# Kernel optimization log

Measured on AMD Instinct MI355X. Metric: run time of the kernel, lower is better.

Reference implementation:

```python
import jax, jax.numpy as jnp
import numpy as np

N_NODES = 100000
N_EDGES = 1600000
H_FEATS = 64


def setup_inputs() -> dict:
    key = jax.random.key(0)
    k_h, k_src, k_dst, k_w1, k_b1, k_w2, k_b2 = jax.random.split(key, 7)
    h = jax.random.normal(k_h, (N_NODES, H_FEATS), dtype=jnp.float32)
    src = jax.random.randint(k_src, (N_EDGES,), 0, N_NODES, dtype=jnp.int64)
    dst = jax.random.randint(k_dst, (N_EDGES,), 0, N_NODES, dtype=jnp.int64)
    # Linear params (torch Linear: y = x @ W.T + b). Store as [in, out] for jnp.
    lim1 = 1.0 / np.sqrt(2 * H_FEATS)
    W1 = jax.random.uniform(k_w1, (2 * H_FEATS, H_FEATS), minval=-lim1, maxval=lim1, dtype=jnp.float32)
    b1 = jax.random.uniform(k_b1, (H_FEATS,), minval=-lim1, maxval=lim1, dtype=jnp.float32)
    lim2 = 1.0 / np.sqrt(H_FEATS)
    W2 = jax.random.uniform(k_w2, (H_FEATS, 1), minval=-lim2, maxval=lim2, dtype=jnp.float32)
    b2 = jax.random.uniform(k_b2, (1,), minval=-lim2, maxval=lim2, dtype=jnp.float32)
    return {"h": h, "src": src, "dst": dst, "W1": W1, "b1": b1, "W2": W2, "b2": b2}


def reference(h, src, dst, W1, b1, W2, b2):
    # Gather src/dst node features per edge, avoid materializing the concat by
    # splitting W1 into the src-half and dst-half of the contraction.
    W1s, W1d = W1[:H_FEATS], W1[H_FEATS:]            # each [h, h]
    h_src = h[src]                                    # [E, h]
    h_dst = h[dst]                                    # [E, h]
    hidden = jax.nn.relu(h_src @ W1s + h_dst @ W1d + b1)  # [E, h]
    score = (hidden @ W2 + b2)[:, 0]                  # [E]
    return score
```

## Files before the change

kernel.cpp:

```cpp
#include <hip/hip_runtime.h>
#include <hip/hip_fp16.h>


#define HF  64
#define PAD 65
#define TN  128

__global__ __launch_bounds__(512) void node_proj_kernel(
    const float* __restrict__ h, const float* __restrict__ W1,
    const float* __restrict__ b1, __half* __restrict__ P,
    __half* __restrict__ Q, int n_nodes)
{
    __shared__ float hs[TN * PAD];

    const int tid  = threadIdx.x;
    const int lane = tid & 63;
    const int wave = __builtin_amdgcn_readfirstlane(tid >> 6);
    const int c0   = wave * 16;
    const bool isQ = c0 >= 64;
    const int ccol = c0 & 63;

    const float* wbase = W1 + (isQ ? (HF * HF) : 0) + ccol;
    __half* const outh = (isQ ? Q : P) + ccol;

    const int n0 = blockIdx.x * TN;

    {
        const int nrow  = (n_nodes - n0 < TN) ? (n_nodes - n0) : TN;
        const int maxf4 = nrow * 16;
        const float4* hv = (const float4*)(h + (size_t)n0 * HF);
        #pragma unroll
        for (int it = 0; it < 4; ++it) {
            const int idx  = tid + it * 512;
            const int cidx = (idx < maxf4) ? idx : 0;
            const float4 v = hv[cidx];
            const int row = idx >> 4;
            const int c4  = (idx & 15) * 4;
            float* dst = &hs[row * PAD + c4];
            dst[0] = v.x; dst[1] = v.y; dst[2] = v.z; dst[3] = v.w;
        }
    }
    __syncthreads();

    float acc0[16], acc1[16];
    #pragma unroll
    for (int j = 0; j < 16; ++j) {
        const float b = isQ ? 0.0f : b1[ccol + j];
        acc0[j] = b; acc1[j] = b;
    }

    const float* r0 = &hs[lane * PAD];
    const float* r1 = &hs[(lane + 64) * PAD];

    #pragma unroll 4
    for (int k2 = 0; k2 < 32; ++k2) {
        const float a0 = r0[2 * k2], a1 = r0[2 * k2 + 1];
        const float c0v = r1[2 * k2], c1v = r1[2 * k2 + 1];
        const float* wA = wbase + (2 * k2) * HF;
        const float* wB = wbase + (2 * k2 + 1) * HF;
        #pragma unroll
        for (int j = 0; j < 16; ++j) {
            const float wa = wA[j], wb = wB[j];
            acc0[j] = fmaf(a0, wa, acc0[j]);
            acc0[j] = fmaf(a1, wb, acc0[j]);
            acc1[j] = fmaf(c0v, wa, acc1[j]);
            acc1[j] = fmaf(c1v, wb, acc1[j]);
        }
    }

    const int n_a = n0 + lane;
    const int n_b = n0 + lane + 64;
    if (n_a < n_nodes) {
        union { uint4 u[2]; __half2 hh[8]; } pk;
        #pragma unroll
        for (int j = 0; j < 8; ++j)
            pk.hh[j] = __floats2half2_rn(acc0[2 * j], acc0[2 * j + 1]);
        __half* base = outh + (size_t)n_a * HF;
        *(uint4*)(base)     = pk.u[0];
        *(uint4*)(base + 8) = pk.u[1];
    }
    if (n_b < n_nodes) {
        union { uint4 u[2]; __half2 hh[8]; } pk;
        #pragma unroll
        for (int j = 0; j < 8; ++j)
            pk.hh[j] = __floats2half2_rn(acc1[2 * j], acc1[2 * j + 1]);
        __half* base = outh + (size_t)n_b * HF;
        *(uint4*)(base)     = pk.u[0];
        *(uint4*)(base + 8) = pk.u[1];
    }
}

__device__ __forceinline__ float dot8_relu(uint4 pv, uint4 qv, float4 wa, float4 wb) {
    const __half2* ph = (const __half2*)&pv;
    const __half2* qh = (const __half2*)&qv;
    const float2 p0 = __half22float2(ph[0]), q0 = __half22float2(qh[0]);
    const float2 p1 = __half22float2(ph[1]), q1 = __half22float2(qh[1]);
    const float2 p2 = __half22float2(ph[2]), q2 = __half22float2(qh[2]);
    const float2 p3 = __half22float2(ph[3]), q3 = __half22float2(qh[3]);
    float acc = 0.f;
    acc = fmaf(fmaxf(p0.x + q0.x, 0.f), wa.x, acc);
    acc = fmaf(fmaxf(p0.y + q0.y, 0.f), wa.y, acc);
    acc = fmaf(fmaxf(p1.x + q1.x, 0.f), wa.z, acc);
    acc = fmaf(fmaxf(p1.y + q1.y, 0.f), wa.w, acc);
    acc = fmaf(fmaxf(p2.x + q2.x, 0.f), wb.x, acc);
    acc = fmaf(fmaxf(p2.y + q2.y, 0.f), wb.y, acc);
    acc = fmaf(fmaxf(p3.x + q3.x, 0.f), wb.z, acc);
    acc = fmaf(fmaxf(p3.y + q3.y, 0.f), wb.w, acc);
    return acc;
}

__device__ __forceinline__ float red8(float v) {
    v += __shfl_xor(v, 4, 8);
    v += __shfl_xor(v, 2, 8);
    v += __shfl_xor(v, 1, 8);
    return v;
}

__global__ __launch_bounds__(256) void edge_score_kernel(
    const __half* __restrict__ P, const __half* __restrict__ Q,
    const int* __restrict__ src, const int* __restrict__ dst,
    const float* __restrict__ W2, const float* __restrict__ b2,
    float* __restrict__ out, int n_edges)
{
    const int tid   = blockIdx.x * 256 + threadIdx.x;
    const int sub   = threadIdx.x & 7;
    const int group = tid >> 3;
    const int j0    = sub * 8;
    const int e0    = group * 8;
    if (e0 >= n_edges) return;

    const float4 w2a = *(const float4*)(W2 + j0);
    const float4 w2b = *(const float4*)(W2 + j0 + 4);
    const float bias2 = b2[0];

    if (e0 + 8 <= n_edges) {
        const int4 sA = *(const int4*)(src + e0);
        const int4 sB = *(const int4*)(src + e0 + 4);
        const int4 dA = *(const int4*)(dst + e0);
        const int4 dB = *(const int4*)(dst + e0 + 4);

        const uint4 p0 = *(const uint4*)(P + (size_t)sA.x * HF + j0);
        const uint4 p1 = *(const uint4*)(P + (size_t)sA.y * HF + j0);
        const uint4 p2 = *(const uint4*)(P + (size_t)sA.z * HF + j0);
        const uint4 p3 = *(const uint4*)(P + (size_t)sA.w * HF + j0);
        const uint4 p4 = *(const uint4*)(P + (size_t)sB.x * HF + j0);
        const uint4 p5 = *(const uint4*)(P + (size_t)sB.y * HF + j0);
        const uint4 p6 = *(const uint4*)(P + (size_t)sB.z * HF + j0);
        const uint4 p7 = *(const uint4*)(P + (size_t)sB.w * HF + j0);
        const uint4 q0 = *(const uint4*)(Q + (size_t)dA.x * HF + j0);
        const uint4 q1 = *(const uint4*)(Q + (size_t)dA.y * HF + j0);
        const uint4 q2 = *(const uint4*)(Q + (size_t)dA.z * HF + j0);
        const uint4 q3 = *(const uint4*)(Q + (size_t)dA.w * HF + j0);
        const uint4 q4 = *(const uint4*)(Q + (size_t)dB.x * HF + j0);
        const uint4 q5 = *(const uint4*)(Q + (size_t)dB.y * HF + j0);
        const uint4 q6 = *(const uint4*)(Q + (size_t)dB.z * HF + j0);
        const uint4 q7 = *(const uint4*)(Q + (size_t)dB.w * HF + j0);

        float s0 = red8(dot8_relu(p0, q0, w2a, w2b));
        float s1 = red8(dot8_relu(p1, q1, w2a, w2b));
        float s2 = red8(dot8_relu(p2, q2, w2a, w2b));
        float s3 = red8(dot8_relu(p3, q3, w2a, w2b));
        float s4 = red8(dot8_relu(p4, q4, w2a, w2b));
        float s5 = red8(dot8_relu(p5, q5, w2a, w2b));
        float s6 = red8(dot8_relu(p6, q6, w2a, w2b));
        float s7 = red8(dot8_relu(p7, q7, w2a, w2b));

        if (sub == 0) {
            *(float4*)(out + e0)     = make_float4(s0 + bias2, s1 + bias2,
                                                   s2 + bias2, s3 + bias2);
            *(float4*)(out + e0 + 4) = make_float4(s4 + bias2, s5 + bias2,
                                                   s6 + bias2, s7 + bias2);
        }
    } else {
        for (int e = e0; e < n_edges; ++e) {
            const int s = src[e];
            const int d = dst[e];
            const uint4 pv = *(const uint4*)(P + (size_t)s * HF + j0);
            const uint4 qv = *(const uint4*)(Q + (size_t)d * HF + j0);
            float sc = red8(dot8_relu(pv, qv, w2a, w2b));
            if (sub == 0) out[e] = sc + bias2;
        }
    }
}

extern "C" void kernel_launch(void* const* d_in, const int* in_sizes, int n_in,
                              void* d_out, int out_size, void* d_ws, size_t ws_size,
                              hipStream_t stream) {
    const float* h   = (const float*)d_in[0];
    const int*   src = (const int*)d_in[1];
    const int*   dst = (const int*)d_in[2];
    const float* W1  = (const float*)d_in[3];
    const float* b1  = (const float*)d_in[4];
    const float* W2  = (const float*)d_in[5];
    const float* b2  = (const float*)d_in[6];
    float* out = (float*)d_out;

    const int n_nodes = in_sizes[0] / HF;
    const int n_edges = in_sizes[1];

    __half* P = (__half*)d_ws;
    __half* Q = P + (size_t)n_nodes * HF;

    const int nblocks1 = (n_nodes + TN - 1) / TN;
    node_proj_kernel<<<nblocks1, 512, 0, stream>>>(h, W1, b1, P, Q, n_nodes);

    const int ngroups  = (n_edges + 7) / 8;
    const int nblocks2 = (ngroups + 31) / 32;
    edge_score_kernel<<<nblocks2, 256, 0, stream>>>(P, Q, src, dst, W2, b2, out, n_edges);
}
```

Measured before the change: 156.2 us.

## Halve node tile, cache h row in registers, vectorize LDS accesses

The node projection kernel now handles 64 nodes per block instead of 128, so each lane owns one node and one set of 16 accumulators. The full 64-float h row is loaded into registers with float4 LDS reads, using a padding of 68 so the float4 accesses stay aligned, and the k loop is fully unrolled. This removes the scalar LDS reads and doubles the block count for more parallelism. In exchange it raises register pressure and halves the reuse of each W1 load across nodes. The edge kernel, which likely dominates runtime, is unchanged.

```diff
diff --git a/kernel.cpp b/kernel.cpp
--- a/kernel.cpp
+++ b/kernel.cpp
@@ -3,8 +3,8 @@
 
 
 #define HF  64
-#define PAD 65
-#define TN  128
+#define TN  64
+#define PAD 68
 
 __global__ __launch_bounds__(512) void node_proj_kernel(
     const float* __restrict__ h, const float* __restrict__ W1,
@@ -23,68 +23,56 @@
     const float* wbase = W1 + (isQ ? (HF * HF) : 0) + ccol;
     __half* const outh = (isQ ? Q : P) + ccol;
 
-    const int n0 = blockIdx.x * TN;
+    const int n0   = blockIdx.x * TN;
+    const int nrow = (n_nodes - n0 < TN) ? (n_nodes - n0) : TN;
 
     {
-        const int nrow  = (n_nodes - n0 < TN) ? (n_nodes - n0) : TN;
         const int maxf4 = nrow * 16;
         const float4* hv = (const float4*)(h + (size_t)n0 * HF);
         #pragma unroll
-        for (int it = 0; it < 4; ++it) {
+        for (int it = 0; it < 2; ++it) {
             const int idx  = tid + it * 512;
             const int cidx = (idx < maxf4) ? idx : 0;
             const float4 v = hv[cidx];
             const int row = idx >> 4;
             const int c4  = (idx & 15) * 4;
-            float* dst = &hs[row * PAD + c4];
-            dst[0] = v.x; dst[1] = v.y; dst[2] = v.z; dst[3] = v.w;
+            *(float4*)&hs[row * PAD + c4] = v;
         }
     }
     __syncthreads();
 
-    float acc0[16], acc1[16];
-    #pragma unroll
-    for (int j = 0; j < 16; ++j) {
-        const float b = isQ ? 0.0f : b1[ccol + j];
-        acc0[j] = b; acc1[j] = b;
-    }
-
-    const float* r0 = &hs[lane * PAD];
-    const float* r1 = &hs[(lane + 64) * PAD];
-
-    #pragma unroll 4
-    for (int k2 = 0; k2 < 32; ++k2) {
-        const float a0 = r0[2 * k2], a1 = r0[2 * k2 + 1];
-        const float c0v = r1[2 * k2], c1v = r1[2 * k2 + 1];
-        const float* wA = wbase + (2 * k2) * HF;
-        const float* wB = wbase + (2 * k2 + 1) * HF;
+    float hreg[64];
+    {
+        const float* r = &hs[lane * PAD];
         #pragma unroll
-        for (int j = 0; j < 16; ++j) {
-            const float wa = wA[j], wb = wB[j];
-            acc0[j] = fmaf(a0, wa, acc0[j]);
-            acc0[j] = fmaf(a1, wb, acc0[j]);
-            acc1[j] = fmaf(c0v, wa, acc1[j]);
-            acc1[j] = fmaf(c1v, wb, acc1[j]);
+        for (int k4 = 0; k4 < 16; ++k4) {
+            const float4 v = *(const float4*)(r + k4 * 4);
+            hreg[k4 * 4 + 0] = v.x;
+            hreg[k4 * 4 + 1] = v.y;
+            hreg[k4 * 4 + 2] = v.z;
+            hreg[k4 * 4 + 3] = v.w;
         }
     }
 
-    const int n_a = n0 + lane;
-    const int n_b = n0 + lane + 64;
-    if (n_a < n_nodes) {
+    float acc[16];
+    #pragma unroll
+    for (int j = 0; j < 16; ++j) acc[j] = isQ ? 0.0f : b1[ccol + j];
+
+    #pragma unroll
+    for (int k = 0; k < 64; ++k) {
+        const float a = hreg[k];
+        const float* w = wbase + k * HF;
+        #pragma unroll
+        for (int j = 0; j < 16; ++j)
+            acc[j] = fmaf(a, w[j], acc[j]);
+    }
+
+    if (lane < nrow) {
         union { uint4 u[2]; __half2 hh[8]; } pk;
         #pragma unroll
         for (int j = 0; j < 8; ++j)
-            pk.hh[j] = __floats2half2_rn(acc0[2 * j], acc0[2 * j + 1]);
-        __half* base = outh + (size_t)n_a * HF;
-        *(uint4*)(base)     = pk.u[0];
-        *(uint4*)(base + 8) = pk.u[1];
-    }
-    if (n_b < n_nodes) {
-        union { uint4 u[2]; __half2 hh[8]; } pk;
-        #pragma unroll
-        for (int j = 0; j < 8; ++j)
-            pk.hh[j] = __floats2half2_rn(acc1[2 * j], acc1[2 * j + 1]);
-        __half* base = outh + (size_t)n_b * HF;
+            pk.hh[j] = __floats2half2_rn(acc[2 * j], acc[2 * j + 1]);
+        __half* base = outh + (size_t)(n0 + lane) * HF;
         *(uint4*)(base)     = pk.u[0];
         *(uint4*)(base + 8) = pk.u[1];
     }
```

New measurement: 160.6 us. 2.9% more time.
